# Performance work log

Measured on AMD Instinct MI355X. Metric: run time of the kernel, lower is better.

## Reference

```python
import jax, jax.numpy as jnp
import numpy as np

B, T, D, H = 32, 512, 512, 1024


def setup_inputs() -> dict:
    key = jax.random.key(0)
    k1, k2, k3 = jax.random.split(key, 3)
    X = jax.random.normal(k1, (B, T, D), dtype=jnp.float32)
    # TF GRUCell variables: gates/kernel [D+H, 2H], gates/bias [2H] (init 1.0),
    # candidate/kernel [D+H, H], candidate/bias [H] (init 0.0). Use small random
    # values for a non-degenerate numerical baseline.
    gate_kernel = jax.random.normal(k2, (D + H, 2 * H), dtype=jnp.float32) * 0.02
    gate_bias = jnp.ones((2 * H,), dtype=jnp.float32)
    cand_kernel = jax.random.normal(k3, (D + H, H), dtype=jnp.float32) * 0.02
    cand_bias = jnp.zeros((H,), dtype=jnp.float32)
    return {"X": X, "gate_kernel": gate_kernel, "gate_bias": gate_bias,
            "cand_kernel": cand_kernel, "cand_bias": cand_bias}


def reference(X, gate_kernel, gate_bias, cand_kernel, cand_bias):
    """Static unidirectional GRU (TF GRUCell math), activation=tanh.
    Returns stacked per-step hidden states [B, T, H]; final state is out[:, -1]."""
    h0 = jnp.zeros((X.shape[0], cand_kernel.shape[1]), dtype=X.dtype)

    def step(h, x_t):
        # gates: r (reset), u (update) = sigmoid([x, h] @ Wg + bg)
        gates = jax.nn.sigmoid(jnp.concatenate([x_t, h], axis=-1) @ gate_kernel + gate_bias)
        r, u = jnp.split(gates, 2, axis=-1)
        # candidate: tanh([x, r*h] @ Wc + bc)
        c = jnp.tanh(jnp.concatenate([x_t, r * h], axis=-1) @ cand_kernel + cand_bias)
        h_new = u * h + (1.0 - u) * c
        return h_new, h_new

    _, hs = jax.lax.scan(step, h0, jnp.swapaxes(X, 0, 1))  # hs: [T, B, H]
    return jnp.swapaxes(hs, 0, 1)  # [B, T, H]
```

## Files before the change

kernel.cpp:

```cpp
#include <hip/hip_runtime.h>
#include <hip/hip_bf16.h>

typedef short s8v __attribute__((ext_vector_type(8)));
typedef float f4v __attribute__((ext_vector_type(4)));
typedef unsigned int u4v __attribute__((ext_vector_type(4)));
typedef unsigned int u2v __attribute__((ext_vector_type(2)));

#define NBLK 64
#define TPB 512

constexpr int BB = 32, TT = 512, DD = 512, HH = 1024;
constexpr int KK = DD + HH;
constexpr int PK = KK + 8;
constexpr int PK8 = PK / 8;
constexpr int K8 = KK / 8;

constexpr size_t OFF_WGT = 0;
constexpr size_t SZ_WGT  = (size_t)2 * HH * KK * 2;
constexpr size_t OFF_WCT = OFF_WGT + SZ_WGT;
constexpr size_t SZ_WCT  = (size_t)HH * KK * 2;
constexpr size_t OFF_XBF = OFF_WCT + SZ_WCT;
constexpr size_t SZ_XBF  = (size_t)BB * TT * DD * 2;
constexpr size_t OFF_HPB = OFF_XBF + SZ_XBF;
constexpr size_t SZ_PUB  = (size_t)BB * HH * 2;
constexpr size_t OFF_RPB = OFF_HPB + SZ_PUB;
constexpr size_t OFF_FLG = OFF_RPB + SZ_PUB;
constexpr size_t SZ_FLG  = (size_t)2 * NBLK * 16 * 4;

__global__ void wtr_kernel(const float* __restrict__ in, unsigned short* __restrict__ out, int N) {
    __shared__ float tl[32][33];
    int tx = threadIdx.x & 31, ty = threadIdx.x >> 5;
    int n0 = blockIdx.x * 32, k0 = blockIdx.y * 32;
#pragma unroll
    for (int r = ty; r < 32; r += 8) tl[r][tx] = in[(size_t)(k0 + r) * N + n0 + tx];
    __syncthreads();
#pragma unroll
    for (int r = ty; r < 32; r += 8) {
        __hip_bfloat16 h = __float2bfloat16(tl[tx][r]);
        out[(size_t)(n0 + r) * KK + k0 + tx] = *reinterpret_cast<unsigned short*>(&h);
    }
}

__global__ void xconv_kernel(const float* __restrict__ X, unsigned short* __restrict__ Xbf) {
    size_t i = ((size_t)blockIdx.x * 256 + threadIdx.x) * 4;
    float4 v = *reinterpret_cast<const float4*>(X + i);
    __hip_bfloat16 h0 = __float2bfloat16(v.x), h1 = __float2bfloat16(v.y);
    __hip_bfloat16 h2 = __float2bfloat16(v.z), h3 = __float2bfloat16(v.w);
    ushort4 o;
    o.x = *(unsigned short*)&h0; o.y = *(unsigned short*)&h1;
    o.z = *(unsigned short*)&h2; o.w = *(unsigned short*)&h3;
    *reinterpret_cast<ushort4*>(Xbf + i) = o;
}

__device__ __forceinline__ u4v cload16(const void* p) {
    u4v r; asm volatile("global_load_dwordx4 %0, %1, off sc0 sc1" : "=v"(r) : "v"(p) : "memory"); return r;
}
__device__ __forceinline__ void cstore8(void* p, u2v v) {
    asm volatile("global_store_dwordx2 %0, %1, off sc0 sc1" :: "v"(p), "v"(v) : "memory");
}
#define B16(x) __builtin_bit_cast(s8v, (x))
#define WAIT_VM(n) do { asm volatile("s_waitcnt vmcnt(" #n ")" ::: "memory"); \
                        __builtin_amdgcn_sched_barrier(0); } while (0)

__device__ __forceinline__ void wait_flags(int* f, int gen) {
    if (threadIdx.x < NBLK) {
        while (__hip_atomic_load(&f[threadIdx.x * 16], __ATOMIC_RELAXED,
                                 __HIP_MEMORY_SCOPE_AGENT) < gen) {
            __builtin_amdgcn_s_sleep(1);
        }
    }
    __syncthreads();
    asm volatile("" ::: "memory");
}

#define MFMA(A, B, C) __builtin_amdgcn_mfma_f32_16x16x32_bf16((A), (B), (C), 0, 0, 0)

__global__ __launch_bounds__(TPB, 1) void gru_kernel(
    const unsigned short* __restrict__ Xbf,
    const unsigned short* __restrict__ WgT,
    const unsigned short* __restrict__ WcT,
    const float* __restrict__ bg,
    const float* __restrict__ bc,
    float* __restrict__ out,
    unsigned short* __restrict__ hpub,
    unsigned short* __restrict__ rpub,
    int* __restrict__ gflagA,
    int* __restrict__ gflagB)
{
    __shared__ unsigned short sWg[32 * PK];
    __shared__ unsigned short sWc[16 * PK];
    __shared__ float sP[2][2][2][16][17];
    __shared__ unsigned short sSRH[32][16];
    __shared__ unsigned short sSH[32][16];

    const int b    = blockIdx.x;
    const int tid  = threadIdx.x;
    const int wid  = tid >> 6;
    const int lane = tid & 63;
    const int l15  = lane & 15;
    const int lq   = lane >> 4;
    const int rt   = wid >> 2;
    const int ks   = wid & 3;
    const int roff = rt * 16;
    const int arow = roff + l15;
    const int bcol0= b * 16;

    {
        s8v* dst = (s8v*)sWg;
        for (int idx = tid; idx < 32 * K8; idx += TPB) {
            int c = idx / K8, k8 = idx % K8;
            int gc = (c < 16) ? (bcol0 + c) : (HH + bcol0 + (c - 16));
            dst[c * PK8 + k8] = ((const s8v*)(WgT + (size_t)gc * KK))[k8];
        }
        s8v* dst2 = (s8v*)sWc;
        for (int idx = tid; idx < 16 * K8; idx += TPB) {
            int c = idx / K8, k8 = idx % K8;
            dst2[c * PK8 + k8] = ((const s8v*)(WcT + (size_t)(bcol0 + c) * KK))[k8];
        }
    }

    const float bgr = bg[bcol0 + l15];
    const float bgu = bg[HH + bcol0 + l15];
    const float bcv = bc[bcol0 + l15];
    const int   ccol = bcol0 + l15;

    const s8v* sWg8 = (const s8v*)sWg;
    const s8v* sWc8 = (const s8v*)sWc;
    const s8v* bwr = sWg8 + l15 * PK8 + lq;
    const s8v* bwu = sWg8 + (16 + l15) * PK8 + lq;
    const s8v* bwc = sWc8 + l15 * PK8 + lq;
    const s8v* bwrx = bwr + 16 * ks;
    const s8v* bwux = bwu + 16 * ks;
    const s8v* bwrh = bwr + 64 + 32 * ks;
    const s8v* bwuh = bwu + 64 + 32 * ks;
    const s8v* bwcx = bwc + 16 * ks;
    const s8v* bwch = bwc + 64 + 32 * ks;

    float hprev[4] = {0.f, 0.f, 0.f, 0.f};
    float ureg[4]  = {0.f, 0.f, 0.f, 0.f};

    __syncthreads();

#pragma unroll 1
    for (int t = 0; t < TT; ++t) {
        const s8v* xk = (const s8v*)(Xbf + (size_t)arow * (TT * DD) + (size_t)t * DD) + lq + 16 * ks;

        f4v ar0 = {0,0,0,0}, ar1 = {0,0,0,0}, au0 = {0,0,0,0}, au1 = {0,0,0,0};
        {
            s8v x0 = xk[0], x1 = xk[4], x2 = xk[8], x3 = xk[12];
            ar0 = MFMA(x0, bwrx[0],  ar0); au0 = MFMA(x0, bwux[0],  au0);
            ar1 = MFMA(x1, bwrx[4],  ar1); au1 = MFMA(x1, bwux[4],  au1);
            ar0 = MFMA(x2, bwrx[8],  ar0); au0 = MFMA(x2, bwux[8],  au0);
            ar1 = MFMA(x3, bwrx[12], ar1); au1 = MFMA(x3, bwux[12], au1);
        }

        if (t > 0) {
            wait_flags(gflagB, t);
            WAIT_VM(0);
            const unsigned short* hp = hpub + (size_t)arow * HH + ks * 256 + lq * 8;
            u4v hb[8];
#pragma unroll
            for (int j = 0; j < 8; ++j) hb[j] = cload16(hp + (size_t)j * 32);
            WAIT_VM(4);
            ar0 = MFMA(B16(hb[0]), bwrh[0],  ar0); au0 = MFMA(B16(hb[0]), bwuh[0],  au0);
            ar1 = MFMA(B16(hb[1]), bwrh[4],  ar1); au1 = MFMA(B16(hb[1]), bwuh[4],  au1);
            ar0 = MFMA(B16(hb[2]), bwrh[8],  ar0); au0 = MFMA(B16(hb[2]), bwuh[8],  au0);
            ar1 = MFMA(B16(hb[3]), bwrh[12], ar1); au1 = MFMA(B16(hb[3]), bwuh[12], au1);
            WAIT_VM(0);
            ar0 = MFMA(B16(hb[4]), bwrh[16], ar0); au0 = MFMA(B16(hb[4]), bwuh[16], au0);
            ar1 = MFMA(B16(hb[5]), bwrh[20], ar1); au1 = MFMA(B16(hb[5]), bwuh[20], au1);
            ar0 = MFMA(B16(hb[6]), bwrh[24], ar0); au0 = MFMA(B16(hb[6]), bwuh[24], au0);
            ar1 = MFMA(B16(hb[7]), bwrh[28], ar1); au1 = MFMA(B16(hb[7]), bwuh[28], au1);
        }

        f4v pr = ar0 + ar1, pu = au0 + au1;
        if (ks & 1) {
            int sl = ks >> 1;
#pragma unroll
            for (int i = 0; i < 4; ++i) {
                sP[sl][rt][0][lq * 4 + i][l15] = pr[i];
                sP[sl][rt][1][lq * 4 + i][l15] = pu[i];
            }
        }
        __syncthreads();
        if (!(ks & 1)) {
            int sl = ks >> 1;
#pragma unroll
            for (int i = 0; i < 4; ++i) {
                pr[i] += sP[sl][rt][0][lq * 4 + i][l15];
                pu[i] += sP[sl][rt][1][lq * 4 + i][l15];
            }
        }
        if (ks == 2) {
#pragma unroll
            for (int i = 0; i < 4; ++i) {
                sP[1][rt][0][lq * 4 + i][l15] = pr[i];
                sP[1][rt][1][lq * 4 + i][l15] = pu[i];
            }
        }
        __syncthreads();
        if (ks == 0) {
#pragma unroll
            for (int i = 0; i < 4; ++i) {
                float zr = pr[i] + sP[1][rt][0][lq * 4 + i][l15] + bgr;
                float zu = pu[i] + sP[1][rt][1][lq * 4 + i][l15] + bgu;
                float r = 1.f / (1.f + __expf(-zr));
                ureg[i] = 1.f / (1.f + __expf(-zu));
                __hip_bfloat16 hb16 = __float2bfloat16(r * hprev[i]);
                sSRH[roff + lq * 4 + i][l15] = *(unsigned short*)&hb16;
            }
        }
        __syncthreads();
        if (t > 0) {
            if (tid < 128) {
                int row = tid >> 2, c4 = (tid & 3) << 2;
                u2v v = *reinterpret_cast<const u2v*>(&sSRH[row][c4]);
                cstore8(rpub + (size_t)row * HH + bcol0 + c4, v);
            }
            asm volatile("s_waitcnt vmcnt(0)" ::: "memory");
            __syncthreads();
            if (tid == 0)
                __hip_atomic_store(&gflagA[b * 16], t, __ATOMIC_RELAXED, __HIP_MEMORY_SCOPE_AGENT);
        }

        f4v c0 = {0,0,0,0}, c1 = {0,0,0,0};
        {
            s8v x0 = xk[0], x1 = xk[4], x2 = xk[8], x3 = xk[12];
            c0 = MFMA(x0, bwcx[0],  c0); c1 = MFMA(x1, bwcx[4],  c1);
            c0 = MFMA(x2, bwcx[8],  c0); c1 = MFMA(x3, bwcx[12], c1);
        }

        if (t > 0) {
            wait_flags(gflagA, t);
            WAIT_VM(0);
            const unsigned short* rp = rpub + (size_t)arow * HH + ks * 256 + lq * 8;
            u4v rb[8];
#pragma unroll
            for (int j = 0; j < 8; ++j) rb[j] = cload16(rp + (size_t)j * 32);
            WAIT_VM(4);
            c0 = MFMA(B16(rb[0]), bwch[0],  c0); c1 = MFMA(B16(rb[1]), bwch[4],  c1);
            c0 = MFMA(B16(rb[2]), bwch[8],  c0); c1 = MFMA(B16(rb[3]), bwch[12], c1);
            WAIT_VM(0);
            c0 = MFMA(B16(rb[4]), bwch[16], c0); c1 = MFMA(B16(rb[5]), bwch[20], c1);
            c0 = MFMA(B16(rb[6]), bwch[24], c0); c1 = MFMA(B16(rb[7]), bwch[28], c1);
        }

        f4v pc = c0 + c1;
        if (ks & 1) {
            int sl = ks >> 1;
#pragma unroll
            for (int i = 0; i < 4; ++i) sP[sl][rt][0][lq * 4 + i][l15] = pc[i];
        }
        __syncthreads();
        if (!(ks & 1)) {
            int sl = ks >> 1;
#pragma unroll
            for (int i = 0; i < 4; ++i) pc[i] += sP[sl][rt][0][lq * 4 + i][l15];
        }
        if (ks == 2) {
#pragma unroll
            for (int i = 0; i < 4; ++i) sP[1][rt][0][lq * 4 + i][l15] = pc[i];
        }
        __syncthreads();
        if (ks == 0) {
#pragma unroll
            for (int i = 0; i < 4; ++i) {
                int row = roff + lq * 4 + i;
                float z = pc[i] + sP[1][rt][0][lq * 4 + i][l15] + bcv;
                float e = __expf(2.f * z);
                float cv = 1.f - 2.f / (e + 1.f);
                float hn = ureg[i] * hprev[i] + (1.f - ureg[i]) * cv;
                out[(size_t)row * (TT * HH) + (size_t)t * HH + ccol] = hn;
                __hip_bfloat16 hb16 = __float2bfloat16(hn);
                sSH[row][l15] = *(unsigned short*)&hb16;
                hprev[i] = hn;
            }
        }
        __syncthreads();
        if (tid < 128) {
            int row = tid >> 2, c4 = (tid & 3) << 2;
            u2v v = *reinterpret_cast<const u2v*>(&sSH[row][c4]);
            cstore8(hpub + (size_t)row * HH + bcol0 + c4, v);
        }
        asm volatile("s_waitcnt vmcnt(0)" ::: "memory");
        __syncthreads();
        if (tid == 0)
            __hip_atomic_store(&gflagB[b * 16], t + 1, __ATOMIC_RELAXED, __HIP_MEMORY_SCOPE_AGENT);
    }
}

extern "C" void kernel_launch(void* const* d_in, const int* in_sizes, int n_in,
                              void* d_out, int out_size, void* d_ws, size_t ws_size,
                              hipStream_t stream) {
    const float* X  = (const float*)d_in[0];
    const float* gk = (const float*)d_in[1];
    const float* gb = (const float*)d_in[2];
    const float* ck = (const float*)d_in[3];
    const float* cb = (const float*)d_in[4];
    float* out = (float*)d_out;
    char* ws = (char*)d_ws;
    if (ws_size < OFF_FLG + SZ_FLG) return;

    unsigned short* WgT  = (unsigned short*)(ws + OFF_WGT);
    unsigned short* WcT  = (unsigned short*)(ws + OFF_WCT);
    unsigned short* Xbf  = (unsigned short*)(ws + OFF_XBF);
    unsigned short* hpub = (unsigned short*)(ws + OFF_HPB);
    unsigned short* rpub = (unsigned short*)(ws + OFF_RPB);
    int*            gflagA = (int*)(ws + OFF_FLG);
    int*            gflagB = gflagA + NBLK * 16;

    hipMemsetAsync(gflagA, 0, SZ_FLG, stream);

    dim3 tb(256);
    wtr_kernel<<<dim3(2 * HH / 32, KK / 32), tb, 0, stream>>>(gk, WgT, 2 * HH);
    wtr_kernel<<<dim3(HH / 32, KK / 32), tb, 0, stream>>>(ck, WcT, HH);
    xconv_kernel<<<(BB * TT * DD) / (256 * 4), tb, 0, stream>>>(X, Xbf);

    gru_kernel<<<NBLK, dim3(TPB), 0, stream>>>(Xbf, WgT, WcT, gb, cb, out,
                                               hpub, rpub, gflagA, gflagB);
}
```

Baseline: 4.541 ms.

## Replace block-wide flag barriers with per-wave, per-row-tile producer polling

The grid flags are split per (block, row-tile). Each wave now polls only the 16 producer blocks whose hidden columns it actually reads, instead of waiting on all 64 blocks and then hitting a __syncthreads. Publishing r*h and h is done by the ks==0 wave of each row tile directly, with no extra block barriers. The reduction across k-slices becomes a single-stage 4-way LDS sum, and the fp32 output store is moved after the flag release so it stays off the critical path. This cuts barrier count and cross-block latency per timestep, at the cost of more subtle intra-wave LDS ordering and more flag memory.

```diff
diff --git a/kernel.cpp b/kernel.cpp
--- a/kernel.cpp
+++ b/kernel.cpp
@@ -25,7 +25,7 @@
 constexpr size_t SZ_PUB  = (size_t)BB * HH * 2;
 constexpr size_t OFF_RPB = OFF_HPB + SZ_PUB;
 constexpr size_t OFF_FLG = OFF_RPB + SZ_PUB;
-constexpr size_t SZ_FLG  = (size_t)2 * NBLK * 16 * 4;
+constexpr size_t SZ_FLG  = (size_t)2 * NBLK * 2 * 16 * 4;
 
 __global__ void wtr_kernel(const float* __restrict__ in, unsigned short* __restrict__ out, int N) {
     __shared__ float tl[32][33];
@@ -62,14 +62,12 @@
 #define WAIT_VM(n) do { asm volatile("s_waitcnt vmcnt(" #n ")" ::: "memory"); \
                         __builtin_amdgcn_sched_barrier(0); } while (0)
 
-__device__ __forceinline__ void wait_flags(int* f, int gen) {
-    if (threadIdx.x < NBLK) {
-        while (__hip_atomic_load(&f[threadIdx.x * 16], __ATOMIC_RELAXED,
-                                 __HIP_MEMORY_SCOPE_AGENT) < gen) {
+__device__ __forceinline__ void poll16(const int* f, int blk0, int rtw, int gen, int lane) {
+    if (lane < 16) {
+        const int* fp = f + ((size_t)(blk0 + lane) * 2 + rtw) * 16;
+        while (__hip_atomic_load(fp, __ATOMIC_RELAXED, __HIP_MEMORY_SCOPE_AGENT) < gen)
             __builtin_amdgcn_s_sleep(1);
-        }
     }
-    __syncthreads();
     asm volatile("" ::: "memory");
 }
 
@@ -89,9 +87,8 @@
 {
     __shared__ unsigned short sWg[32 * PK];
     __shared__ unsigned short sWc[16 * PK];
-    __shared__ float sP[2][2][2][16][17];
-    __shared__ unsigned short sSRH[32][16];
-    __shared__ unsigned short sSH[32][16];
+    __shared__ float sP[3][2][2][16][16];
+    __shared__ unsigned short sStage[32][16];
 
     const int b    = blockIdx.x;
     const int tid  = threadIdx.x;
@@ -99,8 +96,8 @@
     const int lane = tid & 63;
     const int l15  = lane & 15;
     const int lq   = lane >> 4;
-    const int rt   = wid >> 2;
-    const int ks   = wid & 3;
+    const int ks   = wid >> 1;
+    const int rt   = wid & 1;
     const int roff = rt * 16;
     const int arow = roff + l15;
     const int bcol0= b * 16;
@@ -155,8 +152,7 @@
         }
 
         if (t > 0) {
-            wait_flags(gflagB, t);
-            WAIT_VM(0);
+            poll16(gflagB, ks * 16, rt, t, lane);
             const unsigned short* hp = hpub + (size_t)arow * HH + ks * 256 + lq * 8;
             u4v hb[8];
 #pragma unroll
@@ -174,53 +170,43 @@
         }
 
         f4v pr = ar0 + ar1, pu = au0 + au1;
-        if (ks & 1) {
-            int sl = ks >> 1;
-#pragma unroll
-            for (int i = 0; i < 4; ++i) {
-                sP[sl][rt][0][lq * 4 + i][l15] = pr[i];
-                sP[sl][rt][1][lq * 4 + i][l15] = pu[i];
+        if (ks > 0) {
+#pragma unroll
+            for (int i = 0; i < 4; ++i) {
+                sP[ks - 1][rt][0][lq * 4 + i][l15] = pr[i];
+                sP[ks - 1][rt][1][lq * 4 + i][l15] = pu[i];
             }
         }
         __syncthreads();
-        if (!(ks & 1)) {
-            int sl = ks >> 1;
-#pragma unroll
-            for (int i = 0; i < 4; ++i) {
-                pr[i] += sP[sl][rt][0][lq * 4 + i][l15];
-                pu[i] += sP[sl][rt][1][lq * 4 + i][l15];
-            }
-        }
-        if (ks == 2) {
-#pragma unroll
-            for (int i = 0; i < 4; ++i) {
-                sP[1][rt][0][lq * 4 + i][l15] = pr[i];
-                sP[1][rt][1][lq * 4 + i][l15] = pu[i];
+        float zr[4], zu[4];
+        if (ks == 0) {
+#pragma unroll
+            for (int i = 0; i < 4; ++i) {
+                int rr = lq * 4 + i;
+                zr[i] = pr[i] + sP[0][rt][0][rr][l15] + sP[1][rt][0][rr][l15]
+                              + sP[2][rt][0][rr][l15] + bgr;
+                zu[i] = pu[i] + sP[0][rt][1][rr][l15] + sP[1][rt][1][rr][l15]
+                              + sP[2][rt][1][rr][l15] + bgu;
             }
         }
         __syncthreads();
         if (ks == 0) {
 #pragma unroll
             for (int i = 0; i < 4; ++i) {
-                float zr = pr[i] + sP[1][rt][0][lq * 4 + i][l15] + bgr;
-                float zu = pu[i] + sP[1][rt][1][lq * 4 + i][l15] + bgu;
-                float r = 1.f / (1.f + __expf(-zr));
-                ureg[i] = 1.f / (1.f + __expf(-zu));
+                float r = 1.f / (1.f + __expf(-zr[i]));
+                ureg[i] = 1.f / (1.f + __expf(-zu[i]));
                 __hip_bfloat16 hb16 = __float2bfloat16(r * hprev[i]);
-                sSRH[roff + lq * 4 + i][l15] = *(unsigned short*)&hb16;
-            }
-        }
-        __syncthreads();
-        if (t > 0) {
-            if (tid < 128) {
-                int row = tid >> 2, c4 = (tid & 3) << 2;
-                u2v v = *reinterpret_cast<const u2v*>(&sSRH[row][c4]);
-                cstore8(rpub + (size_t)row * HH + bcol0 + c4, v);
-            }
-            asm volatile("s_waitcnt vmcnt(0)" ::: "memory");
-            __syncthreads();
-            if (tid == 0)
-                __hip_atomic_store(&gflagA[b * 16], t, __ATOMIC_RELAXED, __HIP_MEMORY_SCOPE_AGENT);
+                sStage[roff + lq * 4 + i][l15] = *(unsigned short*)&hb16;
+            }
+            if (t > 0) {
+                int prow = roff + (lane >> 2), pc4 = (lane & 3) * 4;
+                u2v v = *reinterpret_cast<const u2v*>(&sStage[prow][pc4]);
+                cstore8(rpub + (size_t)prow * HH + bcol0 + pc4, v);
+                asm volatile("s_waitcnt vmcnt(0)" ::: "memory");
+                if (lane == 0)
+                    __hip_atomic_store(&gflagA[(b * 2 + rt) * 16], t,
+                                       __ATOMIC_RELAXED, __HIP_MEMORY_SCOPE_AGENT);
+            }
         }
 
         f4v c0 = {0,0,0,0}, c1 = {0,0,0,0};
@@ -231,8 +217,7 @@
         }
 
         if (t > 0) {
-            wait_flags(gflagA, t);
-            WAIT_VM(0);
+            poll16(gflagA, ks * 16, rt, t, lane);
             const unsigned short* rp = rpub + (size_t)arow * HH + ks * 256 + lq * 8;
             u4v rb[8];
 #pragma unroll
@@ -246,46 +231,44 @@
         }
 
         f4v pc = c0 + c1;
-        if (ks & 1) {
-            int sl = ks >> 1;
-#pragma unroll
-            for (int i = 0; i < 4; ++i) sP[sl][rt][0][lq * 4 + i][l15] = pc[i];
+        if (ks > 0) {
+#pragma unroll
+            for (int i = 0; i < 4; ++i) sP[ks - 1][rt][0][lq * 4 + i][l15] = pc[i];
         }
         __syncthreads();
-        if (!(ks & 1)) {
-            int sl = ks >> 1;
-#pragma unroll
-            for (int i = 0; i < 4; ++i) pc[i] += sP[sl][rt][0][lq * 4 + i][l15];
-        }
-        if (ks == 2) {
-#pragma unroll
-            for (int i = 0; i < 4; ++i) sP[1][rt][0][lq * 4 + i][l15] = pc[i];
+        float zc[4];
+        if (ks == 0) {
+#pragma unroll
+            for (int i = 0; i < 4; ++i) {
+                int rr = lq * 4 + i;
+                zc[i] = pc[i] + sP[0][rt][0][rr][l15] + sP[1][rt][0][rr][l15]
+                              + sP[2][rt][0][rr][l15] + bcv;
+            }
         }
         __syncthreads();
         if (ks == 0) {
 #pragma unroll
             for (int i = 0; i < 4; ++i) {
-                int row = roff + lq * 4 + i;
-                float z = pc[i] + sP[1][rt][0][lq * 4 + i][l15] + bcv;
-                float e = __expf(2.f * z);
+                float e = __expf(2.f * zc[i]);
                 float cv = 1.f - 2.f / (e + 1.f);
                 float hn = ureg[i] * hprev[i] + (1.f - ureg[i]) * cv;
-                out[(size_t)row * (TT * HH) + (size_t)t * HH + ccol] = hn;
+                hprev[i] = hn;
                 __hip_bfloat16 hb16 = __float2bfloat16(hn);
-                sSH[row][l15] = *(unsigned short*)&hb16;
-                hprev[i] = hn;
-            }
-        }
-        __syncthreads();
-        if (tid < 128) {
-            int row = tid >> 2, c4 = (tid & 3) << 2;
-            u2v v = *reinterpret_cast<const u2v*>(&sSH[row][c4]);
-            cstore8(hpub + (size_t)row * HH + bcol0 + c4, v);
-        }
-        asm volatile("s_waitcnt vmcnt(0)" ::: "memory");
-        __syncthreads();
-        if (tid == 0)
-            __hip_atomic_store(&gflagB[b * 16], t + 1, __ATOMIC_RELAXED, __HIP_MEMORY_SCOPE_AGENT);
+                sStage[roff + lq * 4 + i][l15] = *(unsigned short*)&hb16;
+            }
+            int prow = roff + (lane >> 2), pc4 = (lane & 3) * 4;
+            u2v v = *reinterpret_cast<const u2v*>(&sStage[prow][pc4]);
+            cstore8(hpub + (size_t)prow * HH + bcol0 + pc4, v);
+            asm volatile("s_waitcnt vmcnt(0)" ::: "memory");
+            if (lane == 0)
+                __hip_atomic_store(&gflagB[(b * 2 + rt) * 16], t + 1,
+                                   __ATOMIC_RELAXED, __HIP_MEMORY_SCOPE_AGENT);
+#pragma unroll
+            for (int i = 0; i < 4; ++i) {
+                int row = roff + lq * 4 + i;
+                out[(size_t)row * (TT * HH) + (size_t)t * HH + ccol] = hprev[i];
+            }
+        }
     }
 }
 
@@ -307,7 +290,7 @@
     unsigned short* hpub = (unsigned short*)(ws + OFF_HPB);
     unsigned short* rpub = (unsigned short*)(ws + OFF_RPB);
     int*            gflagA = (int*)(ws + OFF_FLG);
-    int*            gflagB = gflagA + NBLK * 16;
+    int*            gflagB = gflagA + NBLK * 2 * 16;
 
     hipMemsetAsync(gflagA, 0, SZ_FLG, stream);
 
```

Result: faster. 3.914 ms (-13.8%).
